# Optimization experiments

Measured on AMD Instinct MI355X. Metric: run time of the kernel, lower is better.

Reference implementation:

```python
import jax, jax.numpy as jnp
import numpy as np

N_SRC, M, K, H = 100000, 20000, 32, 128
NEG_SLOPE = 0.01  # torch LeakyReLU default


def setup_inputs() -> dict:
    key = jax.random.key(0)
    ks = jax.random.split(key, 8)
    nei = jax.random.randint(ks[0], (M, K), 0, N_SRC)
    h = jax.random.normal(ks[1], (N_SRC, 1), dtype=jnp.float32)
    h_refer = jax.random.normal(ks[2], (M, 1), dtype=jnp.float32)
    # map_l / map_r: Linear(1, H), weight init U[0,1), bias U[0,0.01)
    map_l_w = jax.random.uniform(ks[3], (H, 1), dtype=jnp.float32)
    map_l_b = jax.random.uniform(ks[4], (H,), dtype=jnp.float32) * 0.01
    map_r_w = jax.random.uniform(ks[5], (H, 1), dtype=jnp.float32)
    map_r_b = jax.random.uniform(ks[6], (H,), dtype=jnp.float32) * 0.01
    # att_inter: xavier_normal gain=1.414 on shape (1, 2H)
    std = 1.414 * np.sqrt(2.0 / (1 + 2 * H))
    att_inter = jax.random.normal(ks[7], (1, 2 * H), dtype=jnp.float32) * std
    return {"nei": nei, "h": h, "h_refer": h_refer,
            "map_l_w": map_l_w, "map_l_b": map_l_b,
            "map_r_w": map_r_w, "map_r_b": map_r_b,
            "att_inter": att_inter}


def reference(nei, h, h_refer, map_l_w, map_l_b, map_r_w, map_r_b, att_inter):
    # project scalar features to H dims
    h = jax.nn.relu(h @ map_l_w.T + map_l_b)            # [N, H]
    hr = jax.nn.relu(h_refer @ map_r_w.T + map_r_b)     # [M, H]
    nei_emb = h[nei]                                    # [M, K, H] gather
    # split attention vector to avoid materializing concat([hr, nei_emb])
    a_ref = att_inter[0, :H]                            # [H]
    a_nei = att_inter[0, H:]                            # [H]
    logits = (hr @ a_ref)[:, None] + nei_emb @ a_nei    # [M, K]
    logits = jnp.where(logits >= 0, logits, NEG_SLOPE * logits)  # leakyrelu
    att = jax.nn.softmax(logits, axis=1)                # softmax over neighbors
    lr_inner = jnp.einsum('mkh,mh->mk', nei_emb, hr)    # [M, K]
    out = jax.nn.relu(jnp.sum(att * lr_inner, axis=1, keepdims=True))  # [M, 1]
    return (out, att)
```

## Files before the change

### kernel.cpp

```cpp
#include <hip/hip_runtime.h>

#define N_SRC 100000
#define M_NODES 20000
#define K_NEI 32
#define H_DIM 128
#define NEG_SLOPE 0.01f

#define BLK_M 32
#define HR_PAD 132

__global__ __launch_bounds__(256) void intra_att_kernel(
    const int*   __restrict__ nei,
    const float* __restrict__ h,
    const float* __restrict__ h_refer,
    const float* __restrict__ map_l_w,
    const float* __restrict__ map_l_b,
    const float* __restrict__ map_r_w,
    const float* __restrict__ map_r_b,
    const float* __restrict__ att_inter,
    float*       __restrict__ out,
    float*       __restrict__ att)
{
    __shared__ __attribute__((aligned(16))) float s_wl[H_DIM];
    __shared__ __attribute__((aligned(16))) float s_bl[H_DIM];
    __shared__ __attribute__((aligned(16))) float s_an[H_DIM];
    __shared__ __attribute__((aligned(16))) float s_hr[BLK_M][HR_PAD];

    const int tid  = threadIdx.x;
    const int slot = tid >> 3;
    const int sub  = tid & 7;
    const int m    = blockIdx.x * BLK_M + slot;

    const int4 nv = *(const int4*)(nei + m * K_NEI + sub * 4);
    float h_i[4];
    h_i[0] = h[nv.x]; h_i[1] = h[nv.y]; h_i[2] = h[nv.z]; h_i[3] = h[nv.w];

    if (tid < H_DIM) {
        s_wl[tid] = map_l_w[tid];
        s_bl[tid] = map_l_b[tid];
        s_an[tid] = att_inter[H_DIM + tid];
    }

    const float rm = h_refer[m];
    float hrdot = 0.f;
    {
        const int jb = sub * 16;
        #pragma unroll
        for (int c = 0; c < 16; c += 4) {
            const float4 wr4 = *(const float4*)(map_r_w + jb + c);
            const float4 br4 = *(const float4*)(map_r_b + jb + c);
            const float4 ar4 = *(const float4*)(att_inter + jb + c);
            float4 hr4;
            hr4.x = fmaxf(0.f, fmaf(rm, wr4.x, br4.x));
            hr4.y = fmaxf(0.f, fmaf(rm, wr4.y, br4.y));
            hr4.z = fmaxf(0.f, fmaf(rm, wr4.z, br4.z));
            hr4.w = fmaxf(0.f, fmaf(rm, wr4.w, br4.w));
            *(float4*)(&s_hr[slot][jb + c]) = hr4;
            hrdot += hr4.x*ar4.x + hr4.y*ar4.y + hr4.z*ar4.z + hr4.w*ar4.w;
        }
        #pragma unroll
        for (int o = 4; o >= 1; o >>= 1) hrdot += __shfl_xor(hrdot, o);
    }
    __syncthreads();

    float lg[4] = {0.f, 0.f, 0.f, 0.f};
    float in_[4] = {0.f, 0.f, 0.f, 0.f};
    const float* hrp = s_hr[slot];
    #pragma unroll 8
    for (int j = 0; j < H_DIM; j += 4) {
        const float4 wl4 = *(const float4*)(s_wl + j);
        const float4 bl4 = *(const float4*)(s_bl + j);
        const float4 an4 = *(const float4*)(s_an + j);
        const float4 hr4 = *(const float4*)(hrp + j);
        #pragma unroll
        for (int t = 0; t < 4; ++t) {
            const float hi = h_i[t];
            const float e0 = fmaxf(0.f, fmaf(hi, wl4.x, bl4.x));
            const float e1 = fmaxf(0.f, fmaf(hi, wl4.y, bl4.y));
            const float e2 = fmaxf(0.f, fmaf(hi, wl4.z, bl4.z));
            const float e3 = fmaxf(0.f, fmaf(hi, wl4.w, bl4.w));
            lg[t] = fmaf(e0, an4.x, lg[t]);
            lg[t] = fmaf(e1, an4.y, lg[t]);
            lg[t] = fmaf(e2, an4.z, lg[t]);
            lg[t] = fmaf(e3, an4.w, lg[t]);
            in_[t] = fmaf(e0, hr4.x, in_[t]);
            in_[t] = fmaf(e1, hr4.y, in_[t]);
            in_[t] = fmaf(e2, hr4.z, in_[t]);
            in_[t] = fmaf(e3, hr4.w, in_[t]);
        }
    }

    #pragma unroll
    for (int t = 0; t < 4; ++t) {
        float l = lg[t] + hrdot;
        lg[t] = (l >= 0.f) ? l : NEG_SLOPE * l;
    }

    float mx = fmaxf(fmaxf(lg[0], lg[1]), fmaxf(lg[2], lg[3]));
    #pragma unroll
    for (int o = 4; o >= 1; o >>= 1) mx = fmaxf(mx, __shfl_xor(mx, o));

    float e[4];
    #pragma unroll
    for (int t = 0; t < 4; ++t) e[t] = __expf(lg[t] - mx);
    float se  = e[0] + e[1] + e[2] + e[3];
    float sei = e[0]*in_[0] + e[1]*in_[1] + e[2]*in_[2] + e[3]*in_[3];
    #pragma unroll
    for (int o = 4; o >= 1; o >>= 1) {
        se  += __shfl_xor(se,  o);
        sei += __shfl_xor(sei, o);
    }

    const float inv = 1.0f / se;
    float4 a4;
    a4.x = e[0] * inv; a4.y = e[1] * inv; a4.z = e[2] * inv; a4.w = e[3] * inv;
    *(float4*)(att + m * K_NEI + sub * 4) = a4;
    if (sub == 0) out[m] = fmaxf(0.f, sei * inv);
}

extern "C" void kernel_launch(void* const* d_in, const int* in_sizes, int n_in,
                              void* d_out, int out_size, void* d_ws, size_t ws_size,
                              hipStream_t stream) {
    const int*   nei       = (const int*)  d_in[0];
    const float* h         = (const float*)d_in[1];
    const float* h_refer   = (const float*)d_in[2];
    const float* map_l_w   = (const float*)d_in[3];
    const float* map_l_b   = (const float*)d_in[4];
    const float* map_r_w   = (const float*)d_in[5];
    const float* map_r_b   = (const float*)d_in[6];
    const float* att_inter = (const float*)d_in[7];

    float* out = (float*)d_out;
    float* att = out + M_NODES;

    const int blocks = M_NODES / BLK_M;
    intra_att_kernel<<<blocks, 256, 0, stream>>>(
        nei, h, h_refer, map_l_w, map_l_b, map_r_w, map_r_b, att_inter,
        out, att);
}
```

Baseline: 19.03 us.

## Split H dimension across thread pairs with 8 neighbors per thread

Each row is now handled by 8 threads arranged as 4 neighbor groups by 2 H-halves. Each thread computes 8 neighbors over 64 channels, and the two halves are combined with one cross-lane shuffle. Blocks shrink to 128 threads covering 16 rows. The intent is to reuse each shared-memory weight load across more neighbors, cutting LDS traffic per FMA, and to issue more gather loads per thread before the barrier. In exchange it adds registers, extra shuffles for the partial sums, and half the threads stay idle during the att stores.

```diff
diff --git a/kernel.cpp b/kernel.cpp
--- a/kernel.cpp
+++ b/kernel.cpp
@@ -6,10 +6,11 @@
 #define H_DIM 128
 #define NEG_SLOPE 0.01f
 
-#define BLK_M 32
+#define BLK_M 16
 #define HR_PAD 132
+#define TASKS 8
 
-__global__ __launch_bounds__(256) void intra_att_kernel(
+__global__ __launch_bounds__(128) void intra_att_kernel(
     const int*   __restrict__ nei,
     const float* __restrict__ h,
     const float* __restrict__ h_refer,
@@ -28,23 +29,22 @@
 
     const int tid  = threadIdx.x;
     const int slot = tid >> 3;
-    const int sub  = tid & 7;
+    const int subj = (tid >> 2) & 1;
+    const int subk = tid & 3;
     const int m    = blockIdx.x * BLK_M + slot;
 
-    const int4 nv = *(const int4*)(nei + m * K_NEI + sub * 4);
-    float h_i[4];
-    h_i[0] = h[nv.x]; h_i[1] = h[nv.y]; h_i[2] = h[nv.z]; h_i[3] = h[nv.w];
+    const int nb = m * K_NEI + subk * TASKS;
+    const int4 nv0 = *(const int4*)(nei + nb);
+    const int4 nv1 = *(const int4*)(nei + nb + 4);
 
-    if (tid < H_DIM) {
-        s_wl[tid] = map_l_w[tid];
-        s_bl[tid] = map_l_b[tid];
-        s_an[tid] = att_inter[H_DIM + tid];
-    }
+    s_wl[tid] = map_l_w[tid];
+    s_bl[tid] = map_l_b[tid];
+    s_an[tid] = att_inter[H_DIM + tid];
 
     const float rm = h_refer[m];
     float hrdot = 0.f;
     {
-        const int jb = sub * 16;
+        const int jb = (tid & 7) * 16;
         #pragma unroll
         for (int c = 0; c < 16; c += 4) {
             const float4 wr4 = *(const float4*)(map_r_w + jb + c);
@@ -58,31 +58,40 @@
             *(float4*)(&s_hr[slot][jb + c]) = hr4;
             hrdot += hr4.x*ar4.x + hr4.y*ar4.y + hr4.z*ar4.z + hr4.w*ar4.w;
         }
-        #pragma unroll
-        for (int o = 4; o >= 1; o >>= 1) hrdot += __shfl_xor(hrdot, o);
+        hrdot += __shfl_xor(hrdot, 1);
+        hrdot += __shfl_xor(hrdot, 2);
+        hrdot += __shfl_xor(hrdot, 4);
     }
+
+    float h_i[TASKS];
+    h_i[0] = h[nv0.x]; h_i[1] = h[nv0.y]; h_i[2] = h[nv0.z]; h_i[3] = h[nv0.w];
+    h_i[4] = h[nv1.x]; h_i[5] = h[nv1.y]; h_i[6] = h[nv1.z]; h_i[7] = h[nv1.w];
+
     __syncthreads();
 
-    float lg[4] = {0.f, 0.f, 0.f, 0.f};
-    float in_[4] = {0.f, 0.f, 0.f, 0.f};
-    const float* hrp = s_hr[slot];
-    #pragma unroll 8
-    for (int j = 0; j < H_DIM; j += 4) {
-        const float4 wl4 = *(const float4*)(s_wl + j);
-        const float4 bl4 = *(const float4*)(s_bl + j);
-        const float4 an4 = *(const float4*)(s_an + j);
-        const float4 hr4 = *(const float4*)(hrp + j);
+    float lg[TASKS]  = {0.f,0.f,0.f,0.f,0.f,0.f,0.f,0.f};
+    float in_[TASKS] = {0.f,0.f,0.f,0.f,0.f,0.f,0.f,0.f};
+    const float* hrp = s_hr[slot] + subj * 64;
+    const float* wlp = s_wl + subj * 64;
+    const float* blp = s_bl + subj * 64;
+    const float* anp = s_an + subj * 64;
+    #pragma unroll 4
+    for (int c = 0; c < 64; c += 4) {
+        const float4 wl4 = *(const float4*)(wlp + c);
+        const float4 bl4 = *(const float4*)(blp + c);
+        const float4 an4 = *(const float4*)(anp + c);
+        const float4 hr4 = *(const float4*)(hrp + c);
         #pragma unroll
-        for (int t = 0; t < 4; ++t) {
+        for (int t = 0; t < TASKS; ++t) {
             const float hi = h_i[t];
             const float e0 = fmaxf(0.f, fmaf(hi, wl4.x, bl4.x));
             const float e1 = fmaxf(0.f, fmaf(hi, wl4.y, bl4.y));
             const float e2 = fmaxf(0.f, fmaf(hi, wl4.z, bl4.z));
             const float e3 = fmaxf(0.f, fmaf(hi, wl4.w, bl4.w));
-            lg[t] = fmaf(e0, an4.x, lg[t]);
-            lg[t] = fmaf(e1, an4.y, lg[t]);
-            lg[t] = fmaf(e2, an4.z, lg[t]);
-            lg[t] = fmaf(e3, an4.w, lg[t]);
+            lg[t]  = fmaf(e0, an4.x, lg[t]);
+            lg[t]  = fmaf(e1, an4.y, lg[t]);
+            lg[t]  = fmaf(e2, an4.z, lg[t]);
+            lg[t]  = fmaf(e3, an4.w, lg[t]);
             in_[t] = fmaf(e0, hr4.x, in_[t]);
             in_[t] = fmaf(e1, hr4.y, in_[t]);
             in_[t] = fmaf(e2, hr4.z, in_[t]);
@@ -91,31 +100,46 @@
     }
 
     #pragma unroll
-    for (int t = 0; t < 4; ++t) {
-        float l = lg[t] + hrdot;
+    for (int t = 0; t < TASKS; ++t) {
+        lg[t]  += __shfl_xor(lg[t],  4);
+        in_[t] += __shfl_xor(in_[t], 4);
+    }
+
+    #pragma unroll
+    for (int t = 0; t < TASKS; ++t) {
+        const float l = lg[t] + hrdot;
         lg[t] = (l >= 0.f) ? l : NEG_SLOPE * l;
     }
 
-    float mx = fmaxf(fmaxf(lg[0], lg[1]), fmaxf(lg[2], lg[3]));
+    float mx = lg[0];
     #pragma unroll
-    for (int o = 4; o >= 1; o >>= 1) mx = fmaxf(mx, __shfl_xor(mx, o));
+    for (int t = 1; t < TASKS; ++t) mx = fmaxf(mx, lg[t]);
+    mx = fmaxf(mx, __shfl_xor(mx, 1));
+    mx = fmaxf(mx, __shfl_xor(mx, 2));
 
-    float e[4];
+    float e[TASKS];
+    float se = 0.f, sei = 0.f;
     #pragma unroll
-    for (int t = 0; t < 4; ++t) e[t] = __expf(lg[t] - mx);
-    float se  = e[0] + e[1] + e[2] + e[3];
-    float sei = e[0]*in_[0] + e[1]*in_[1] + e[2]*in_[2] + e[3]*in_[3];
-    #pragma unroll
-    for (int o = 4; o >= 1; o >>= 1) {
-        se  += __shfl_xor(se,  o);
-        sei += __shfl_xor(sei, o);
+    for (int t = 0; t < TASKS; ++t) {
+        e[t] = __expf(lg[t] - mx);
+        se  += e[t];
+        sei += e[t] * in_[t];
     }
+    se  += __shfl_xor(se,  1);
+    se  += __shfl_xor(se,  2);
+    sei += __shfl_xor(sei, 1);
+    sei += __shfl_xor(sei, 2);
 
     const float inv = 1.0f / se;
-    float4 a4;
-    a4.x = e[0] * inv; a4.y = e[1] * inv; a4.z = e[2] * inv; a4.w = e[3] * inv;
-    *(float4*)(att + m * K_NEI + sub * 4) = a4;
-    if (sub == 0) out[m] = fmaxf(0.f, sei * inv);
+    if (subj == 0) {
+        float4 a0, a1;
+        a0.x = e[0]*inv; a0.y = e[1]*inv; a0.z = e[2]*inv; a0.w = e[3]*inv;
+        a1.x = e[4]*inv; a1.y = e[5]*inv; a1.z = e[6]*inv; a1.w = e[7]*inv;
+        float* ap = att + m * K_NEI + subk * TASKS;
+        *(float4*)(ap)     = a0;
+        *(float4*)(ap + 4) = a1;
+        if (subk == 0) out[m] = fmaxf(0.f, sei * inv);
+    }
 }
 
 extern "C" void kernel_launch(void* const* d_in, const int* in_sizes, int n_in,
@@ -134,7 +158,7 @@
     float* att = out + M_NODES;
 
     const int blocks = M_NODES / BLK_M;
-    intra_att_kernel<<<blocks, 256, 0, stream>>>(
+    intra_att_kernel<<<blocks, 128, 0, stream>>>(
         nei, h, h_refer, map_l_w, map_l_b, map_r_w, map_r_b, att_inter,
         out, att);
 }
```

Measured after the change: 19.90 us. +4.6%, slower.

## Replace per-neighbor H-dim dot products with piecewise-linear breakpoint lookup

Applied to the files above, without the earlier changes.

Because each neighbor embedding is relu(x*w+b) of a scalar, both the logit and the inner product are piecewise-linear in x with breakpoints at -b/w. A prep kernel sorts the breakpoints and builds prefix sums of slope and intercept for the attention vector. The main kernel builds per-row prefix sums for hr, then binary-searches each neighbor's scalar to evaluate both quantities in O(log H) instead of O(H). This adds a second tiny launch and a workspace dependency, and it assumes map_l_w is positive.

```diff
diff --git a/kernel.cpp b/kernel.cpp
--- a/kernel.cpp
+++ b/kernel.cpp
@@ -6,116 +6,202 @@
 #define H_DIM 128
 #define NEG_SLOPE 0.01f
 
-#define BLK_M 32
-#define HR_PAD 132
-
-__global__ __launch_bounds__(256) void intra_att_kernel(
-    const int*   __restrict__ nei,
-    const float* __restrict__ h,
-    const float* __restrict__ h_refer,
+#define WS_T    0
+#define WS_WL   128
+#define WS_BL   256
+#define WS_WR   384
+#define WS_BR   512
+#define WS_AR   640
+#define WS_SA   768
+
+__global__ __launch_bounds__(128) void prep_kernel(
     const float* __restrict__ map_l_w,
     const float* __restrict__ map_l_b,
     const float* __restrict__ map_r_w,
     const float* __restrict__ map_r_b,
     const float* __restrict__ att_inter,
+    float* __restrict__ ws)
+{
+    __shared__ float s_t[H_DIM];
+    __shared__ int   s_ord[H_DIM];
+    __shared__ float s_cw[H_DIM];
+    __shared__ float s_cb[H_DIM];
+
+    const int j = threadIdx.x;
+    const float wl = map_l_w[j];
+    const float bl = map_l_b[j];
+    const float t  = -bl / fmaxf(wl, 1e-30f);
+    s_t[j] = t;
+    __syncthreads();
+
+    int rank = 0;
+    #pragma unroll 8
+    for (int i = 0; i < H_DIM; ++i) {
+        const float ti = s_t[i];
+        rank += (ti < t || (ti == t && i < j)) ? 1 : 0;
+    }
+    s_ord[rank] = j;
+    __syncthreads();
+
+    const int src = s_ord[j];
+    const float wls = map_l_w[src];
+    const float bls = map_l_b[src];
+    ws[WS_T  + j] = s_t[src];
+    ws[WS_WL + j] = wls;
+    ws[WS_BL + j] = bls;
+    ws[WS_WR + j] = map_r_w[src];
+    ws[WS_BR + j] = map_r_b[src];
+    ws[WS_AR + j] = att_inter[src];
+    const float an = att_inter[H_DIM + src];
+    s_cw[j] = an * wls;
+    s_cb[j] = an * bls;
+    __syncthreads();
+
+    if (j < 8) {
+        const int sb = j * 16;
+        float cw[16], cb[16];
+        float sw = 0.f, sbv = 0.f;
+        #pragma unroll
+        for (int i = 0; i < 16; ++i) {
+            cw[i] = s_cw[sb + i]; cb[i] = s_cb[sb + i];
+            sw += cw[i]; sbv += cb[i];
+        }
+        float iw = sw, ib = sbv, v;
+        v = __shfl_up(iw, 1); if (j >= 1) iw += v;
+        v = __shfl_up(ib, 1); if (j >= 1) ib += v;
+        v = __shfl_up(iw, 2); if (j >= 2) iw += v;
+        v = __shfl_up(ib, 2); if (j >= 2) ib += v;
+        v = __shfl_up(iw, 4); if (j >= 4) iw += v;
+        v = __shfl_up(ib, 4); if (j >= 4) ib += v;
+        float rw = iw - sw, rb = ib - sbv;
+        float2* sa = (float2*)(ws + WS_SA);
+        #pragma unroll
+        for (int i = 0; i < 16; ++i) {
+            sa[sb + i] = make_float2(rw, rb);
+            rw += cw[i]; rb += cb[i];
+        }
+        if (j == 7) sa[H_DIM] = make_float2(rw, rb);
+    }
+}
+
+#define BLK_M2 16
+#define SH_STRIDE 132
+
+__global__ __launch_bounds__(128) void main_kernel(
+    const int*   __restrict__ nei,
+    const float* __restrict__ h,
+    const float* __restrict__ h_refer,
+    const float* __restrict__ ws,
     float*       __restrict__ out,
     float*       __restrict__ att)
 {
-    __shared__ __attribute__((aligned(16))) float s_wl[H_DIM];
-    __shared__ __attribute__((aligned(16))) float s_bl[H_DIM];
-    __shared__ __attribute__((aligned(16))) float s_an[H_DIM];
-    __shared__ __attribute__((aligned(16))) float s_hr[BLK_M][HR_PAD];
+    __shared__ float  s_T[H_DIM];
+    __shared__ float2 s_SA[H_DIM + 1];
+    __shared__ float2 s_SH[BLK_M2][SH_STRIDE];
 
     const int tid  = threadIdx.x;
     const int slot = tid >> 3;
-    const int sub  = tid & 7;
-    const int m    = blockIdx.x * BLK_M + slot;
-
-    const int4 nv = *(const int4*)(nei + m * K_NEI + sub * 4);
-    float h_i[4];
-    h_i[0] = h[nv.x]; h_i[1] = h[nv.y]; h_i[2] = h[nv.z]; h_i[3] = h[nv.w];
+    const int u    = tid & 7;
+    const int m    = blockIdx.x * BLK_M2 + slot;
+
+    const int4  nv = *(const int4*)(nei + m * K_NEI + u * 4);
+    const float rm = h_refer[m];
 
     if (tid < H_DIM) {
-        s_wl[tid] = map_l_w[tid];
-        s_bl[tid] = map_l_b[tid];
-        s_an[tid] = att_inter[H_DIM + tid];
-    }
-
-    const float rm = h_refer[m];
+        s_T[tid]  = ws[WS_T + tid];
+        s_SA[tid] = ((const float2*)(ws + WS_SA))[tid];
+    }
+    if (tid == 0) s_SA[H_DIM] = ((const float2*)(ws + WS_SA))[H_DIM];
+
+    const float x0 = h[nv.x], x1 = h[nv.y], x2 = h[nv.z], x3 = h[nv.w];
+
+    const int sb = u * 16;
     float hrdot = 0.f;
+    float cw[16], cb[16];
+    float sw = 0.f, sbv = 0.f;
+    #pragma unroll
+    for (int q = 0; q < 4; ++q) {
+        const float4 wr4 = *(const float4*)(ws + WS_WR + sb + q * 4);
+        const float4 br4 = *(const float4*)(ws + WS_BR + sb + q * 4);
+        const float4 ar4 = *(const float4*)(ws + WS_AR + sb + q * 4);
+        const float4 wl4 = *(const float4*)(ws + WS_WL + sb + q * 4);
+        const float4 bl4 = *(const float4*)(ws + WS_BL + sb + q * 4);
+        const float h0 = fmaxf(0.f, fmaf(rm, wr4.x, br4.x));
+        const float h1 = fmaxf(0.f, fmaf(rm, wr4.y, br4.y));
+        const float h2 = fmaxf(0.f, fmaf(rm, wr4.z, br4.z));
+        const float h3 = fmaxf(0.f, fmaf(rm, wr4.w, br4.w));
+        hrdot += h0*ar4.x + h1*ar4.y + h2*ar4.z + h3*ar4.w;
+        cw[q*4+0] = h0*wl4.x; cb[q*4+0] = h0*bl4.x;
+        cw[q*4+1] = h1*wl4.y; cb[q*4+1] = h1*bl4.y;
+        cw[q*4+2] = h2*wl4.z; cb[q*4+2] = h2*bl4.z;
+        cw[q*4+3] = h3*wl4.w; cb[q*4+3] = h3*bl4.w;
+        sw  += cw[q*4+0] + cw[q*4+1] + cw[q*4+2] + cw[q*4+3];
+        sbv += cb[q*4+0] + cb[q*4+1] + cb[q*4+2] + cb[q*4+3];
+    }
     {
-        const int jb = sub * 16;
+        float iw = sw, ib = sbv, v;
+        v = __shfl_up(iw, 1); if (u >= 1) iw += v;
+        v = __shfl_up(ib, 1); if (u >= 1) ib += v;
+        v = __shfl_up(iw, 2); if (u >= 2) iw += v;
+        v = __shfl_up(ib, 2); if (u >= 2) ib += v;
+        v = __shfl_up(iw, 4); if (u >= 4) iw += v;
+        v = __shfl_up(ib, 4); if (u >= 4) ib += v;
+        float rw = iw - sw, rb = ib - sbv;
         #pragma unroll
-        for (int c = 0; c < 16; c += 4) {
-            const float4 wr4 = *(const float4*)(map_r_w + jb + c);
-            const float4 br4 = *(const float4*)(map_r_b + jb + c);
-            const float4 ar4 = *(const float4*)(att_inter + jb + c);
-            float4 hr4;
-            hr4.x = fmaxf(0.f, fmaf(rm, wr4.x, br4.x));
-            hr4.y = fmaxf(0.f, fmaf(rm, wr4.y, br4.y));
-            hr4.z = fmaxf(0.f, fmaf(rm, wr4.z, br4.z));
-            hr4.w = fmaxf(0.f, fmaf(rm, wr4.w, br4.w));
-            *(float4*)(&s_hr[slot][jb + c]) = hr4;
-            hrdot += hr4.x*ar4.x + hr4.y*ar4.y + hr4.z*ar4.z + hr4.w*ar4.w;
+        for (int q = 0; q < 8; ++q) {
+            float4 t4;
+            t4.x = rw; t4.y = rb; rw += cw[q*2];   rb += cb[q*2];
+            t4.z = rw; t4.w = rb; rw += cw[q*2+1]; rb += cb[q*2+1];
+            *(float4*)(&s_SH[slot][sb + q*2]) = t4;
         }
-        #pragma unroll
-        for (int o = 4; o >= 1; o >>= 1) hrdot += __shfl_xor(hrdot, o);
-    }
-    __syncthreads();
-
-    float lg[4] = {0.f, 0.f, 0.f, 0.f};
-    float in_[4] = {0.f, 0.f, 0.f, 0.f};
-    const float* hrp = s_hr[slot];
-    #pragma unroll 8
-    for (int j = 0; j < H_DIM; j += 4) {
-        const float4 wl4 = *(const float4*)(s_wl + j);
-        const float4 bl4 = *(const float4*)(s_bl + j);
-        const float4 an4 = *(const float4*)(s_an + j);
-        const float4 hr4 = *(const float4*)(hrp + j);
-        #pragma unroll
-        for (int t = 0; t < 4; ++t) {
-            const float hi = h_i[t];
-            const float e0 = fmaxf(0.f, fmaf(hi, wl4.x, bl4.x));
-            const float e1 = fmaxf(0.f, fmaf(hi, wl4.y, bl4.y));
-            const float e2 = fmaxf(0.f, fmaf(hi, wl4.z, bl4.z));
-            const float e3 = fmaxf(0.f, fmaf(hi, wl4.w, bl4.w));
-            lg[t] = fmaf(e0, an4.x, lg[t]);
-            lg[t] = fmaf(e1, an4.y, lg[t]);
-            lg[t] = fmaf(e2, an4.z, lg[t]);
-            lg[t] = fmaf(e3, an4.w, lg[t]);
-            in_[t] = fmaf(e0, hr4.x, in_[t]);
-            in_[t] = fmaf(e1, hr4.y, in_[t]);
-            in_[t] = fmaf(e2, hr4.z, in_[t]);
-            in_[t] = fmaf(e3, hr4.w, in_[t]);
-        }
-    }
-
+        if (u == 7) s_SH[slot][H_DIM] = make_float2(rw, rb);
+    }
+    hrdot += __shfl_xor(hrdot, 1);
+    hrdot += __shfl_xor(hrdot, 2);
+    hrdot += __shfl_xor(hrdot, 4);
+
+    __syncthreads();
+
+    const float xs[4] = {x0, x1, x2, x3};
+    float lg[4], in_[4];
+    float mx = -3.4e38f;
     #pragma unroll
     for (int t = 0; t < 4; ++t) {
-        float l = lg[t] + hrdot;
-        lg[t] = (l >= 0.f) ? l : NEG_SLOPE * l;
-    }
-
-    float mx = fmaxf(fmaxf(lg[0], lg[1]), fmaxf(lg[2], lg[3]));
+        const float x = xs[t];
+        int r = (s_T[63] < x) ? 64 : 0;
+        if (s_T[r+31] < x) r += 32;
+        if (s_T[r+15] < x) r += 16;
+        if (s_T[r+7]  < x) r += 8;
+        if (s_T[r+3]  < x) r += 4;
+        if (s_T[r+1]  < x) r += 2;
+        if (s_T[r]    < x) r += 1;
+        if (s_T[r]    < x) r += 1;
+        const float2 sa = s_SA[r];
+        const float2 sh = s_SH[slot][r];
+        const float l = fmaf(sa.x, x, sa.y) + hrdot;
+        lg[t]  = (l >= 0.f) ? l : NEG_SLOPE * l;
+        in_[t] = fmaf(sh.x, x, sh.y);
+        mx = fmaxf(mx, lg[t]);
+    }
+    mx = fmaxf(mx, __shfl_xor(mx, 1));
+    mx = fmaxf(mx, __shfl_xor(mx, 2));
+    mx = fmaxf(mx, __shfl_xor(mx, 4));
+
+    float e[4];
+    float se = 0.f, sei = 0.f;
     #pragma unroll
-    for (int o = 4; o >= 1; o >>= 1) mx = fmaxf(mx, __shfl_xor(mx, o));
-
-    float e[4];
-    #pragma unroll
-    for (int t = 0; t < 4; ++t) e[t] = __expf(lg[t] - mx);
-    float se  = e[0] + e[1] + e[2] + e[3];
-    float sei = e[0]*in_[0] + e[1]*in_[1] + e[2]*in_[2] + e[3]*in_[3];
-    #pragma unroll
-    for (int o = 4; o >= 1; o >>= 1) {
-        se  += __shfl_xor(se,  o);
-        sei += __shfl_xor(sei, o);
-    }
+    for (int t = 0; t < 4; ++t) {
+        e[t] = __expf(lg[t] - mx);
+        se  += e[t];
+        sei += e[t] * in_[t];
+    }
+    se  += __shfl_xor(se, 1);  se  += __shfl_xor(se, 2);  se  += __shfl_xor(se, 4);
+    sei += __shfl_xor(sei, 1); sei += __shfl_xor(sei, 2); sei += __shfl_xor(sei, 4);
 
     const float inv = 1.0f / se;
-    float4 a4;
-    a4.x = e[0] * inv; a4.y = e[1] * inv; a4.z = e[2] * inv; a4.w = e[3] * inv;
-    *(float4*)(att + m * K_NEI + sub * 4) = a4;
-    if (sub == 0) out[m] = fmaxf(0.f, sei * inv);
+    const float4 a4 = make_float4(e[0]*inv, e[1]*inv, e[2]*inv, e[3]*inv);
+    *(float4*)(att + m * K_NEI + u * 4) = a4;
+    if (u == 0) out[m] = fmaxf(0.f, sei * inv);
 }
 
 extern "C" void kernel_launch(void* const* d_in, const int* in_sizes, int n_in,
@@ -132,9 +218,12 @@
 
     float* out = (float*)d_out;
     float* att = out + M_NODES;
-
-    const int blocks = M_NODES / BLK_M;
-    intra_att_kernel<<<blocks, 256, 0, stream>>>(
-        nei, h, h_refer, map_l_w, map_l_b, map_r_w, map_r_b, att_inter,
-        out, att);
+    float* ws  = (float*)d_ws;
+
+    prep_kernel<<<1, 128, 0, stream>>>(
+        map_l_w, map_l_b, map_r_w, map_r_b, att_inter, ws);
+
+    const int blocks = M_NODES / BLK_M2;
+    main_kernel<<<blocks, 128, 0, stream>>>(
+        nei, h, h_refer, ws, out, att);
 }
```

Measured after the change: 18.28 us. 1.04x faster.
